# Kernel tuning notes

Hardware: AMD Instinct MI355X
Metric: run time of the kernel (lower is better)

Reference implementation:

```python
import jax, jax.numpy as jnp
import numpy as np

B, T, N, D = 8, 64, 128, 128  # batch, timesteps, num_nodes, hidden_dim
LN_EPS = 1e-5
L2_EPS = 1e-12


def setup_inputs() -> dict:
    key = jax.random.key(0)
    ks = jax.random.split(key, 8)
    feat = jax.random.normal(ks[0], (B, T, N, D), dtype=jnp.float32)
    w = jax.random.uniform(ks[1], (D,), dtype=jnp.float32)  # learned adj gate (torch.rand init)
    s = 1.0 / np.sqrt(D)
    W1 = jax.random.uniform(ks[2], (D, D), dtype=jnp.float32, minval=-s, maxval=s)
    b1 = jax.random.uniform(ks[3], (D,), dtype=jnp.float32, minval=-s, maxval=s)
    W2 = jax.random.uniform(ks[4], (D, D), dtype=jnp.float32, minval=-s, maxval=s)
    b2 = jax.random.uniform(ks[5], (D,), dtype=jnp.float32, minval=-s, maxval=s)
    gamma = jnp.ones((D,), dtype=jnp.float32)
    beta = jnp.zeros((D,), dtype=jnp.float32)
    return {"feat": feat, "w": w, "W1": W1, "b1": b1, "W2": W2, "b2": b2,
            "gamma": gamma, "beta": beta}


def _windows(x):
    # x: (B, T, N, D) -> (B, T-2, 3*N, D): 3 consecutive timesteps flattened over nodes
    b, t, n, d = x.shape
    return jnp.stack([x[:, i:i + t - 2] for i in range(3)], axis=2).reshape(b, t - 2, 3 * n, d)


def reference(feat, w, W1, b1, W2, b2, gamma, beta):
    # gated + L2-normalized features for learned adjacency
    wf = feat * jax.nn.sigmoid(w)
    wf = wf / jnp.maximum(jnp.linalg.norm(wf, axis=-1, keepdims=True), L2_EPS)

    win = _windows(feat)   # (B, T-2, 3N, D)
    wwin = _windows(wf)    # (B, T-2, 3N, D)

    # learned adjacency: gram matrix per window, (B, T-2, 3N, 3N)
    adj = jnp.einsum('btmd,btnd->btmn', wwin, wwin)

    # symmetric normalization D^{-1/2} A D^{-1/2}; inf/nan (deg<=0) -> 0 as in torch
    deg = adj.sum(axis=-1, keepdims=True)
    dis = jnp.where(deg > 0, jax.lax.rsqrt(jnp.maximum(deg, 1e-38)), 0.0)
    nadj = dis * adj * jnp.swapaxes(dis, -1, -2)

    # message passing, keep last N rows (current timestep)
    agg = jnp.einsum('btmn,btnd->btmd', nadj, win)[:, :, -N:, :]

    # FFN (dropout is identity in eval): Linear -> ReLU -> Linear
    h = jax.nn.relu(agg @ W1 + b1) @ W2 + b2

    # residual with current-timestep features + LayerNorm
    s = feat[:, 2:] + h
    mu = s.mean(axis=-1, keepdims=True)
    var = ((s - mu) ** 2).mean(axis=-1, keepdims=True)
    return (s - mu) * jax.lax.rsqrt(var + LN_EPS) * gamma + beta
```

## Files before the change

### kernel.cpp

```cpp
#include <hip/hip_runtime.h>
#include <math.h>

#define BB    8
#define TDIM  64
#define NN    128
#define DD    128
#define TTOUT 62
#define W3    384
#define LG    136
#define LP    40
#define LW    72

typedef __attribute__((ext_vector_type(8))) short bf16x8;
typedef __attribute__((ext_vector_type(4))) float f32x4;

__device__ __forceinline__ float sigf(float x){ return 1.0f/(1.0f+__expf(-x)); }
__device__ __forceinline__ unsigned short f2bf(float x){
  union{float f; unsigned u;} v; v.f=x;
  unsigned r = v.u + 0x7FFFu + ((v.u>>16)&1u);
  return (unsigned short)(r>>16);
}

__global__ void k_rscale(const float* __restrict__ feat, const float* __restrict__ w,
                         float* __restrict__ rscale){
  int row  = blockIdx.x*4 + (threadIdx.x>>6);
  int lane = threadIdx.x & 63;
  float2 f  = *(const float2*)(feat + (size_t)row*DD + lane*2);
  float2 wv = *(const float2*)(w + lane*2);
  float v0 = f.x * sigf(wv.x);
  float v1 = f.y * sigf(wv.y);
  float ss = v0*v0 + v1*v1;
  #pragma unroll
  for(int k=32;k>=1;k>>=1) ss += __shfl_xor(ss, k);
  if(lane==0) rscale[row] = 1.0f / fmaxf(sqrtf(ss), 1e-12f);
}

__global__ void k_ssum(const float* __restrict__ feat, const float* __restrict__ w,
                       const float* __restrict__ rscale, float* __restrict__ ssum){
  int bt = blockIdx.x;
  int d  = threadIdx.x;
  const float* fp = feat + (size_t)bt*NN*DD + d;
  const float* rp = rscale + bt*NN;
  float acc = 0.f;
  #pragma unroll 4
  for(int n=0;n<NN;n++) acc += fp[(size_t)n*DD] * rp[n];
  ssum[bt*DD + d] = acc * sigf(w[d]);
}

__global__ void k_dis(const float* __restrict__ feat, const float* __restrict__ w,
                      const float* __restrict__ rscale, const float* __restrict__ ssum,
                      float* __restrict__ dis){
  __shared__ float s3[DD];
  __shared__ float sg[DD];
  int bt2 = blockIdx.x;
  int b = bt2 / TTOUT, tt = bt2 % TTOUT;
  int tid = threadIdx.x;
  if(tid < DD){
    int base = (b*TDIM + tt)*DD;
    s3[tid] = ssum[base+tid] + ssum[base+DD+tid] + ssum[base+2*DD+tid];
    sg[tid] = sigf(w[tid]);
  }
  __syncthreads();
  int gr = (b*TDIM + tt)*NN + tid;
  const float4* fr = (const float4*)(feat + (size_t)gr*DD);
  float deg = 0.f;
  #pragma unroll 8
  for(int q=0;q<DD/4;q++){
    float4 f = fr[q];
    deg += f.x*sg[q*4+0]*s3[q*4+0] + f.y*sg[q*4+1]*s3[q*4+1]
         + f.z*sg[q*4+2]*s3[q*4+2] + f.w*sg[q*4+3]*s3[q*4+3];
  }
  deg *= rscale[gr];
  dis[(size_t)bt2*W3 + tid] = (deg > 0.f) ? rsqrtf(fmaxf(deg, 1e-38f)) : 0.f;
}

__global__ __launch_bounds__(512,4) void k_main(
    const float* __restrict__ feat,
    const float* __restrict__ W1, const float* __restrict__ b1,
    const float* __restrict__ W2, const float* __restrict__ b2,
    const float* __restrict__ gamma, const float* __restrict__ beta,
    const float* __restrict__ w,
    const float* __restrict__ rscale, const float* __restrict__ dis,
    float* __restrict__ out)
{
  __shared__ __align__(16) unsigned short sm[32000];
  __shared__ float sSig[DD];
  unsigned short* sA  = sm;
  unsigned short* sG  = sm + 17408;
  unsigned short* sFt = sm + 21760;
  unsigned short* sP  = sm + 26880;
  unsigned short* sWt = sm + 17408;

  const int bt2 = blockIdx.x;
  const int tid = threadIdx.x;
  const int rowBase = (bt2/TTOUT)*TDIM*NN + (bt2%TTOUT)*NN;
  const float* disP = dis + (size_t)bt2*W3;

  const int lane = tid & 63, wid = tid >> 6;
  const int l15 = lane & 15, l4 = lane >> 4;
  const int m0 = wid * 16;

  if(tid < DD) sSig[tid] = sigf(w[tid]);
  __syncthreads();

  #pragma unroll
  for(int e0=0; e0<8; ++e0){
    int e = e0*512 + tid;
    int d = e & 127, r0 = (e>>7)*4;
    float sg = sSig[d];
    #pragma unroll
    for(int i=0;i<4;i++){
      int j = 256 + r0 + i, gr = rowBase + j;
      float f = feat[(size_t)gr*DD + d];
      float fac = rscale[gr]*disP[j];
      sA[(r0+i)*LG + d] = f2bf(f*sg*fac);
    }
  }

  f32x4 acc2[8];
  #pragma unroll
  for(int i=0;i<8;i++) acc2[i] = (f32x4){0.f,0.f,0.f,0.f};

  for(int c=0; c<12; ++c){
    const int n0 = c*32;
    __syncthreads();
    #pragma unroll
    for(int e0=0; e0<2; ++e0){
      int e = e0*512 + tid;
      int d = e & 127, r0 = (e>>7)*4;
      float sg = sSig[d];
      unsigned short fb[4];
      #pragma unroll
      for(int i=0;i<4;i++){
        int j = n0 + r0 + i, gr = rowBase + j;
        float f = feat[(size_t)gr*DD + d];
        float fac = rscale[gr]*disP[j];
        fb[i] = f2bf(f);
        sG[(r0+i)*LG + d] = f2bf(f*sg*fac);
      }
      unsigned int* fp = (unsigned int*)&sFt[d*LP + r0];
      fp[0] = (unsigned)fb[0] | ((unsigned)fb[1]<<16);
      fp[1] = (unsigned)fb[2] | ((unsigned)fb[3]<<16);
    }
    __syncthreads();

    f32x4 p0 = {0.f,0.f,0.f,0.f}, p1 = {0.f,0.f,0.f,0.f};
    #pragma unroll
    for(int ks=0; ks<4; ++ks){
      bf16x8 aA  = *(const bf16x8*)&sA[(m0+l15)*LG + ks*32 + l4*8];
      bf16x8 bg0 = *(const bf16x8*)&sG[( 0+l15)*LG + ks*32 + l4*8];
      bf16x8 bg1 = *(const bf16x8*)&sG[(16+l15)*LG + ks*32 + l4*8];
      p0 = __builtin_amdgcn_mfma_f32_16x16x32_bf16(aA, bg0, p0, 0,0,0);
      p1 = __builtin_amdgcn_mfma_f32_16x16x32_bf16(aA, bg1, p1, 0,0,0);
    }
    #pragma unroll
    for(int r=0;r<4;r++){
      sP[(m0 + l4*4 + r)*LP +  0 + l15] = f2bf(p0[r]);
      sP[(m0 + l4*4 + r)*LP + 16 + l15] = f2bf(p1[r]);
    }
    __syncthreads();

    bf16x8 aP = *(const bf16x8*)&sP[(m0+l15)*LP + l4*8];
    #pragma unroll
    for(int dt=0; dt<8; ++dt){
      bf16x8 bF = *(const bf16x8*)&sFt[(dt*16+l15)*LP + l4*8];
      acc2[dt] = __builtin_amdgcn_mfma_f32_16x16x32_bf16(aP, bF, acc2[dt], 0,0,0);
    }
  }

  #pragma unroll
  for(int dt=0; dt<8; ++dt)
    #pragma unroll
    for(int r=0;r<4;r++)
      sA[(m0+l4*4+r)*LG + dt*16+l15] = f2bf(acc2[dt][r]);

  f32x4 acch[8];
  #pragma unroll
  for(int dt=0; dt<8; ++dt){
    float bv = b1[dt*16+l15];
    acch[dt] = (f32x4){bv,bv,bv,bv};
  }
  for(int kh=0; kh<2; ++kh){
    __syncthreads();
    #pragma unroll
    for(int e0=0; e0<4; ++e0){
      int e = e0*512+tid;
      int n = e&127, k0 = (e>>7)*4;
      float w0 = W1[(size_t)(kh*64+k0+0)*DD + n];
      float w1v= W1[(size_t)(kh*64+k0+1)*DD + n];
      float w2v= W1[(size_t)(kh*64+k0+2)*DD + n];
      float w3v= W1[(size_t)(kh*64+k0+3)*DD + n];
      unsigned int* wp = (unsigned int*)&sWt[n*LW + k0];
      wp[0] = (unsigned)f2bf(w0) | ((unsigned)f2bf(w1v)<<16);
      wp[1] = (unsigned)f2bf(w2v)| ((unsigned)f2bf(w3v)<<16);
    }
    __syncthreads();
    #pragma unroll
    for(int ks=0; ks<2; ++ks){
      bf16x8 aA = *(const bf16x8*)&sA[(m0+l15)*LG + kh*64 + ks*32 + l4*8];
      #pragma unroll
      for(int dt=0; dt<8; ++dt){
        bf16x8 bW = *(const bf16x8*)&sWt[(dt*16+l15)*LW + ks*32 + l4*8];
        acch[dt] = __builtin_amdgcn_mfma_f32_16x16x32_bf16(aA, bW, acch[dt], 0,0,0);
      }
    }
  }
  __syncthreads();
  #pragma unroll
  for(int dt=0; dt<8; ++dt)
    #pragma unroll
    for(int r=0;r<4;r++)
      sA[(m0+l4*4+r)*LG + dt*16+l15] = f2bf(fmaxf(acch[dt][r], 0.f));

  f32x4 acco[8];
  #pragma unroll
  for(int dt=0; dt<8; ++dt){
    float bv = b2[dt*16+l15];
    acco[dt] = (f32x4){bv,bv,bv,bv};
  }
  for(int kh=0; kh<2; ++kh){
    __syncthreads();
    #pragma unroll
    for(int e0=0; e0<4; ++e0){
      int e = e0*512+tid;
      int n = e&127, k0 = (e>>7)*4;
      float w0 = W2[(size_t)(kh*64+k0+0)*DD + n];
      float w1v= W2[(size_t)(kh*64+k0+1)*DD + n];
      float w2v= W2[(size_t)(kh*64+k0+2)*DD + n];
      float w3v= W2[(size_t)(kh*64+k0+3)*DD + n];
      unsigned int* wp = (unsigned int*)&sWt[n*LW + k0];
      wp[0] = (unsigned)f2bf(w0) | ((unsigned)f2bf(w1v)<<16);
      wp[1] = (unsigned)f2bf(w2v)| ((unsigned)f2bf(w3v)<<16);
    }
    __syncthreads();
    #pragma unroll
    for(int ks=0; ks<2; ++ks){
      bf16x8 aA = *(const bf16x8*)&sA[(m0+l15)*LG + kh*64 + ks*32 + l4*8];
      #pragma unroll
      for(int dt=0; dt<8; ++dt){
        bf16x8 bW = *(const bf16x8*)&sWt[(dt*16+l15)*LW + ks*32 + l4*8];
        acco[dt] = __builtin_amdgcn_mfma_f32_16x16x32_bf16(aA, bW, acco[dt], 0,0,0);
      }
    }
  }

  const float* fres = feat + (size_t)(rowBase + 256)*DD;
  #pragma unroll
  for(int r=0;r<4;r++){
    int m = m0 + l4*4 + r;
    float vals[8]; float s1 = 0.f, s2 = 0.f;
    #pragma unroll
    for(int dt=0; dt<8; ++dt){
      int d = dt*16 + l15;
      float v = acco[dt][r] + fres[(size_t)m*DD + d];
      vals[dt] = v; s1 += v; s2 += v*v;
    }
    #pragma unroll
    for(int k=1;k<16;k<<=1){ s1 += __shfl_xor(s1,k); s2 += __shfl_xor(s2,k); }
    float mu   = s1*(1.0f/DD);
    float rstd = rsqrtf(s2*(1.0f/DD) - mu*mu + 1e-5f);
    #pragma unroll
    for(int dt=0; dt<8; ++dt){
      int d = dt*16 + l15;
      out[((size_t)bt2*NN + m)*DD + d] = (vals[dt]-mu)*rstd*gamma[d] + beta[d];
    }
  }
}

extern "C" void kernel_launch(void* const* d_in, const int* in_sizes, int n_in,
                              void* d_out, int out_size, void* d_ws, size_t ws_size,
                              hipStream_t stream){
  const float* feat  = (const float*)d_in[0];
  const float* w     = (const float*)d_in[1];
  const float* W1    = (const float*)d_in[2];
  const float* b1    = (const float*)d_in[3];
  const float* W2    = (const float*)d_in[4];
  const float* b2    = (const float*)d_in[5];
  const float* gamma = (const float*)d_in[6];
  const float* beta  = (const float*)d_in[7];
  float* out = (float*)d_out;

  float* rscale = (float*)d_ws;
  float* ssum   = rscale + BB*TDIM*NN;
  float* dis    = ssum   + BB*TDIM*DD;

  k_rscale<<<BB*TDIM*NN/4, 256, 0, stream>>>(feat, w, rscale);
  k_ssum  <<<BB*TDIM,      128, 0, stream>>>(feat, w, rscale, ssum);
  k_dis   <<<BB*TTOUT,     W3,  0, stream>>>(feat, w, rscale, ssum, dis);
  k_main  <<<BB*TTOUT,     512, 0, stream>>>(feat, W1, b1, W2, b2, gamma, beta, w,
                                             rscale, dis, out);
}
```

Measured before the change: 90.92 us.

## Precompute bf16 normalized features and transposed weights; defer degree scaling to Gram output

A fused preprocessing kernel computes the L2 scale, per-timestep column sums and bf16 copies of the gated-normalized features and the raw features in one pass. A separate kernel pre-transposes W1/W2 to bf16, and per-row degree partials over five neighbouring timesteps replace the per-window degree kernel. The main kernel now loads the bf16 tiles with vectorized copies instead of recomputing and converting per element, and applies the D^-1/2 scaling to the Gram block output rather than to the inputs. This adds workspace traffic and extra launches but cuts redundant recomputation across the overlapping windows, at the cost of slightly different rounding.

```diff
diff --git a/kernel.cpp b/kernel.cpp
--- a/kernel.cpp
+++ b/kernel.cpp
@@ -8,7 +8,8 @@
 #define TTOUT 62
 #define W3    384
 #define LG    136
-#define LP    40
+#define LPF   44
+#define LPP   44
 #define LW    72
 
 typedef __attribute__((ext_vector_type(8))) short bf16x8;
@@ -21,100 +22,151 @@
   return (unsigned short)(r>>16);
 }
 
-__global__ void k_rscale(const float* __restrict__ feat, const float* __restrict__ w,
-                         float* __restrict__ rscale){
-  int row  = blockIdx.x*4 + (threadIdx.x>>6);
-  int lane = threadIdx.x & 63;
-  float2 f  = *(const float2*)(feat + (size_t)row*DD + lane*2);
-  float2 wv = *(const float2*)(w + lane*2);
-  float v0 = f.x * sigf(wv.x);
-  float v1 = f.y * sigf(wv.y);
-  float ss = v0*v0 + v1*v1;
-  #pragma unroll
-  for(int k=32;k>=1;k>>=1) ss += __shfl_xor(ss, k);
-  if(lane==0) rscale[row] = 1.0f / fmaxf(sqrtf(ss), 1e-12f);
-}
-
-__global__ void k_ssum(const float* __restrict__ feat, const float* __restrict__ w,
-                       const float* __restrict__ rscale, float* __restrict__ ssum){
-  int bt = blockIdx.x;
-  int d  = threadIdx.x;
-  const float* fp = feat + (size_t)bt*NN*DD + d;
-  const float* rp = rscale + bt*NN;
-  float acc = 0.f;
-  #pragma unroll 4
-  for(int n=0;n<NN;n++) acc += fp[(size_t)n*DD] * rp[n];
-  ssum[bt*DD + d] = acc * sigf(w[d]);
-}
-
-__global__ void k_dis(const float* __restrict__ feat, const float* __restrict__ w,
-                      const float* __restrict__ rscale, const float* __restrict__ ssum,
-                      float* __restrict__ dis){
-  __shared__ float s3[DD];
-  __shared__ float sg[DD];
-  int bt2 = blockIdx.x;
-  int b = bt2 / TTOUT, tt = bt2 % TTOUT;
-  int tid = threadIdx.x;
+template<bool FBF>
+__global__ __launch_bounds__(512) void k_pre(const float* __restrict__ feat,
+    const float* __restrict__ w, unsigned short* __restrict__ gbf,
+    unsigned short* __restrict__ fbf, float* __restrict__ rscale,
+    float* __restrict__ ssum){
+  __shared__ float sSig[DD];
+  __shared__ float sPart[8*DD];
+  const int bt = blockIdx.x, tid = threadIdx.x;
+  if(tid < DD) sSig[tid] = sigf(w[tid]);
+  __syncthreads();
+  const int row = tid >> 2, q = tid & 3;
+  const float* fp = feat + ((size_t)bt*NN + row)*DD + q*32;
+  float f[32], g[32];
+  #pragma unroll
+  for(int i=0;i<8;i++){
+    float4 v = *(const float4*)(fp + i*4);
+    f[i*4]=v.x; f[i*4+1]=v.y; f[i*4+2]=v.z; f[i*4+3]=v.w;
+  }
+  float ss = 0.f;
+  #pragma unroll
+  for(int j=0;j<32;j++){ g[j] = f[j]*sSig[q*32+j]; ss += g[j]*g[j]; }
+  ss += __shfl_xor(ss,1); ss += __shfl_xor(ss,2);
+  float rs = 1.0f / fmaxf(sqrtf(ss), 1e-12f);
+  if(q==0) rscale[(size_t)bt*NN + row] = rs;
+  #pragma unroll
+  for(int j=0;j<32;j++) g[j] *= rs;
+  {
+    unsigned u[16];
+    #pragma unroll
+    for(int j=0;j<16;j++) u[j] = (unsigned)f2bf(g[2*j]) | ((unsigned)f2bf(g[2*j+1])<<16);
+    uint4* dst = (uint4*)(gbf + ((size_t)bt*NN+row)*DD + q*32);
+    #pragma unroll
+    for(int i=0;i<4;i++) dst[i] = *(uint4*)&u[i*4];
+  }
+  if(FBF){
+    unsigned u[16];
+    #pragma unroll
+    for(int j=0;j<16;j++) u[j] = (unsigned)f2bf(f[2*j]) | ((unsigned)f2bf(f[2*j+1])<<16);
+    uint4* dst = (uint4*)(fbf + ((size_t)bt*NN+row)*DD + q*32);
+    #pragma unroll
+    for(int i=0;i<4;i++) dst[i] = *(uint4*)&u[i*4];
+  }
+  #pragma unroll
+  for(int k=4;k<64;k<<=1){
+    #pragma unroll
+    for(int j=0;j<32;j++) g[j] += __shfl_xor(g[j], k);
+  }
+  const int lane = tid & 63, wid = tid >> 6;
+  if((lane>>2)==0){
+    #pragma unroll
+    for(int j=0;j<32;j++) sPart[wid*DD + q*32 + j] = g[j];
+  }
+  __syncthreads();
   if(tid < DD){
-    int base = (b*TDIM + tt)*DD;
-    s3[tid] = ssum[base+tid] + ssum[base+DD+tid] + ssum[base+2*DD+tid];
-    sg[tid] = sigf(w[tid]);
+    float s = 0.f;
+    #pragma unroll
+    for(int wv=0; wv<8; wv++) s += sPart[wv*DD + tid];
+    ssum[(size_t)bt*DD + tid] = s;
+  }
+}
+
+__global__ void k_wt(const float* __restrict__ W1, const float* __restrict__ W2,
+                     unsigned short* __restrict__ W1T, unsigned short* __restrict__ W2T){
+  int k = blockIdx.x & 127, m = blockIdx.x >> 7;
+  int n = threadIdx.x;
+  const float* W = m ? W2 : W1;
+  unsigned short* WT = m ? W2T : W1T;
+  WT[n*DD + k] = f2bf(W[(size_t)k*DD + n]);
+}
+
+__global__ __launch_bounds__(256) void k_d5(const float* __restrict__ feat,
+    const float* __restrict__ w, const float* __restrict__ rscale,
+    const float* __restrict__ ssum, float* __restrict__ d5){
+  __shared__ float s5[5*DD];
+  const int tb = blockIdx.x, tid = threadIdx.x;
+  for(int e=tid; e<5*DD; e+=256){
+    int k = e>>7, d = e&127;
+    int t2 = (tb & 63) - 2 + k;
+    float v = 0.f;
+    if(t2 >= 0 && t2 < TDIM) v = sigf(w[d]) * ssum[(size_t)(tb + k - 2)*DD + d];
+    s5[k*DD + d] = v;
   }
   __syncthreads();
-  int gr = (b*TDIM + tt)*NN + tid;
-  const float4* fr = (const float4*)(feat + (size_t)gr*DD);
-  float deg = 0.f;
-  #pragma unroll 8
-  for(int q=0;q<DD/4;q++){
-    float4 f = fr[q];
-    deg += f.x*sg[q*4+0]*s3[q*4+0] + f.y*sg[q*4+1]*s3[q*4+1]
-         + f.z*sg[q*4+2]*s3[q*4+2] + f.w*sg[q*4+3]*s3[q*4+3];
-  }
-  deg *= rscale[gr];
-  dis[(size_t)bt2*W3 + tid] = (deg > 0.f) ? rsqrtf(fmaxf(deg, 1e-38f)) : 0.f;
-}
-
+  const int row = tid>>1, h = tid&1;
+  const float* fp = feat + ((size_t)tb*NN + row)*DD + h*64;
+  float a0=0,a1=0,a2=0,a3=0,a4=0;
+  #pragma unroll
+  for(int i=0;i<16;i++){
+    float4 v = *(const float4*)(fp + i*4);
+    const float* s0 = s5 + h*64 + i*4;
+    a0 += v.x*s0[0*DD+0] + v.y*s0[0*DD+1] + v.z*s0[0*DD+2] + v.w*s0[0*DD+3];
+    a1 += v.x*s0[1*DD+0] + v.y*s0[1*DD+1] + v.z*s0[1*DD+2] + v.w*s0[1*DD+3];
+    a2 += v.x*s0[2*DD+0] + v.y*s0[2*DD+1] + v.z*s0[2*DD+2] + v.w*s0[2*DD+3];
+    a3 += v.x*s0[3*DD+0] + v.y*s0[3*DD+1] + v.z*s0[3*DD+2] + v.w*s0[3*DD+3];
+    a4 += v.x*s0[4*DD+0] + v.y*s0[4*DD+1] + v.z*s0[4*DD+2] + v.w*s0[4*DD+3];
+  }
+  a0 += __shfl_xor(a0,1); a1 += __shfl_xor(a1,1); a2 += __shfl_xor(a2,1);
+  a3 += __shfl_xor(a3,1); a4 += __shfl_xor(a4,1);
+  if(h==0){
+    float rs = rscale[(size_t)tb*NN + row];
+    float* dp = d5 + ((size_t)tb*NN + row)*5;
+    dp[0]=a0*rs; dp[1]=a1*rs; dp[2]=a2*rs; dp[3]=a3*rs; dp[4]=a4*rs;
+  }
+}
+
+template<bool FBF>
 __global__ __launch_bounds__(512,4) void k_main(
     const float* __restrict__ feat,
-    const float* __restrict__ W1, const float* __restrict__ b1,
-    const float* __restrict__ W2, const float* __restrict__ b2,
+    const unsigned short* __restrict__ gbf,
+    const unsigned short* __restrict__ fbf,
+    const float* __restrict__ d5,
+    const unsigned short* __restrict__ W1T, const float* __restrict__ b1,
+    const unsigned short* __restrict__ W2T, const float* __restrict__ b2,
     const float* __restrict__ gamma, const float* __restrict__ beta,
-    const float* __restrict__ w,
-    const float* __restrict__ rscale, const float* __restrict__ dis,
     float* __restrict__ out)
 {
-  __shared__ __align__(16) unsigned short sm[32000];
-  __shared__ float sSig[DD];
+  __shared__ __align__(16) unsigned short sm[33024];
+  __shared__ float sDis[W3];
   unsigned short* sA  = sm;
   unsigned short* sG  = sm + 17408;
   unsigned short* sFt = sm + 21760;
-  unsigned short* sP  = sm + 26880;
+  unsigned short* sP  = sm + 27392;
   unsigned short* sWt = sm + 17408;
 
   const int bt2 = blockIdx.x;
   const int tid = threadIdx.x;
   const int rowBase = (bt2/TTOUT)*TDIM*NN + (bt2%TTOUT)*NN;
-  const float* disP = dis + (size_t)bt2*W3;
 
   const int lane = tid & 63, wid = tid >> 6;
   const int l15 = lane & 15, l4 = lane >> 4;
   const int m0 = wid * 16;
 
-  if(tid < DD) sSig[tid] = sigf(w[tid]);
-  __syncthreads();
-
-  #pragma unroll
-  for(int e0=0; e0<8; ++e0){
-    int e = e0*512 + tid;
-    int d = e & 127, r0 = (e>>7)*4;
-    float sg = sSig[d];
-    #pragma unroll
-    for(int i=0;i<4;i++){
-      int j = 256 + r0 + i, gr = rowBase + j;
-      float f = feat[(size_t)gr*DD + d];
-      float fac = rscale[gr]*disP[j];
-      sA[(r0+i)*LG + d] = f2bf(f*sg*fac);
-    }
+  if(tid < W3){
+    int jb = tid >> 7;
+    const float* dp = d5 + (size_t)(rowBase + tid)*5 + (2 - jb);
+    float deg = dp[0] + dp[1] + dp[2];
+    sDis[tid] = (deg > 0.f) ? rsqrtf(fmaxf(deg, 1e-38f)) : 0.f;
+  }
+
+  #pragma unroll
+  for(int it=0; it<4; ++it){
+    int e = it*512 + tid;
+    int r = e >> 4, sg = e & 15;
+    uint4 v = *(const uint4*)(gbf + (size_t)(rowBase+256+r)*DD + sg*8);
+    *(uint4*)(sA + r*LG + sg*8) = v;
   }
 
   f32x4 acc2[8];
@@ -124,23 +176,37 @@
   for(int c=0; c<12; ++c){
     const int n0 = c*32;
     __syncthreads();
-    #pragma unroll
-    for(int e0=0; e0<2; ++e0){
-      int e = e0*512 + tid;
-      int d = e & 127, r0 = (e>>7)*4;
-      float sg = sSig[d];
-      unsigned short fb[4];
-      #pragma unroll
-      for(int i=0;i<4;i++){
-        int j = n0 + r0 + i, gr = rowBase + j;
-        float f = feat[(size_t)gr*DD + d];
-        float fac = rscale[gr]*disP[j];
-        fb[i] = f2bf(f);
-        sG[(r0+i)*LG + d] = f2bf(f*sg*fac);
+    {
+      int r = tid >> 4, sg = tid & 15;
+      uint4 v = *(const uint4*)(gbf + (size_t)(rowBase+n0+r)*DD + sg*8);
+      *(uint4*)(sG + r*LG + sg*8) = v;
+    }
+    {
+      int p = tid & 63, rg = tid >> 6;
+      int d0 = p*2, r0 = rg*4;
+      unsigned v0,v1,v2,v3;
+      if(FBF){
+        v0 = *(const unsigned*)(fbf + (size_t)(rowBase+n0+r0+0)*DD + d0);
+        v1 = *(const unsigned*)(fbf + (size_t)(rowBase+n0+r0+1)*DD + d0);
+        v2 = *(const unsigned*)(fbf + (size_t)(rowBase+n0+r0+2)*DD + d0);
+        v3 = *(const unsigned*)(fbf + (size_t)(rowBase+n0+r0+3)*DD + d0);
+      } else {
+        float2 a0 = *(const float2*)(feat + (size_t)(rowBase+n0+r0+0)*DD + d0);
+        float2 a1 = *(const float2*)(feat + (size_t)(rowBase+n0+r0+1)*DD + d0);
+        float2 a2 = *(const float2*)(feat + (size_t)(rowBase+n0+r0+2)*DD + d0);
+        float2 a3 = *(const float2*)(feat + (size_t)(rowBase+n0+r0+3)*DD + d0);
+        v0 = (unsigned)f2bf(a0.x) | ((unsigned)f2bf(a0.y)<<16);
+        v1 = (unsigned)f2bf(a1.x) | ((unsigned)f2bf(a1.y)<<16);
+        v2 = (unsigned)f2bf(a2.x) | ((unsigned)f2bf(a2.y)<<16);
+        v3 = (unsigned)f2bf(a3.x) | ((unsigned)f2bf(a3.y)<<16);
       }
-      unsigned int* fp = (unsigned int*)&sFt[d*LP + r0];
-      fp[0] = (unsigned)fb[0] | ((unsigned)fb[1]<<16);
-      fp[1] = (unsigned)fb[2] | ((unsigned)fb[3]<<16);
+      uint2 lo, hi;
+      lo.x = (v0 & 0xffffu) | (v1 << 16);
+      lo.y = (v2 & 0xffffu) | (v3 << 16);
+      hi.x = (v0 >> 16) | (v1 & 0xffff0000u);
+      hi.y = (v2 >> 16) | (v3 & 0xffff0000u);
+      *(uint2*)(sFt + (size_t)d0*LPF + r0)     = lo;
+      *(uint2*)(sFt + (size_t)(d0+1)*LPF + r0) = hi;
     }
     __syncthreads();
 
@@ -153,17 +219,21 @@
       p0 = __builtin_amdgcn_mfma_f32_16x16x32_bf16(aA, bg0, p0, 0,0,0);
       p1 = __builtin_amdgcn_mfma_f32_16x16x32_bf16(aA, bg1, p1, 0,0,0);
     }
-    #pragma unroll
-    for(int r=0;r<4;r++){
-      sP[(m0 + l4*4 + r)*LP +  0 + l15] = f2bf(p0[r]);
-      sP[(m0 + l4*4 + r)*LP + 16 + l15] = f2bf(p1[r]);
-    }
-    __syncthreads();
-
-    bf16x8 aP = *(const bf16x8*)&sP[(m0+l15)*LP + l4*8];
+    {
+      float dn0 = sDis[n0 + l15], dn1 = sDis[n0 + 16 + l15];
+      #pragma unroll
+      for(int r=0;r<4;r++){
+        float dm = sDis[256 + m0 + l4*4 + r];
+        sP[(m0+l4*4+r)*LPP +  0 + l15] = f2bf(p0[r]*dm*dn0);
+        sP[(m0+l4*4+r)*LPP + 16 + l15] = f2bf(p1[r]*dm*dn1);
+      }
+    }
+    __syncthreads();
+
+    bf16x8 aP = *(const bf16x8*)&sP[(m0+l15)*LPP + l4*8];
     #pragma unroll
     for(int dt=0; dt<8; ++dt){
-      bf16x8 bF = *(const bf16x8*)&sFt[(dt*16+l15)*LP + l4*8];
+      bf16x8 bF = *(const bf16x8*)&sFt[(dt*16+l15)*LPF + l4*8];
       acc2[dt] = __builtin_amdgcn_mfma_f32_16x16x32_bf16(aP, bF, acc2[dt], 0,0,0);
     }
   }
@@ -183,16 +253,11 @@
   for(int kh=0; kh<2; ++kh){
     __syncthreads();
     #pragma unroll
-    for(int e0=0; e0<4; ++e0){
-      int e = e0*512+tid;
-      int n = e&127, k0 = (e>>7)*4;
-      float w0 = W1[(size_t)(kh*64+k0+0)*DD + n];
-      float w1v= W1[(size_t)(kh*64+k0+1)*DD + n];
-      float w2v= W1[(size_t)(kh*64+k0+2)*DD + n];
-      float w3v= W1[(size_t)(kh*64+k0+3)*DD + n];
-      unsigned int* wp = (unsigned int*)&sWt[n*LW + k0];
-      wp[0] = (unsigned)f2bf(w0) | ((unsigned)f2bf(w1v)<<16);
-      wp[1] = (unsigned)f2bf(w2v)| ((unsigned)f2bf(w3v)<<16);
+    for(int it=0; it<2; ++it){
+      int e = it*512 + tid;
+      int n = e>>3, sg = e&7;
+      uint4 v = *(const uint4*)(W1T + (size_t)n*DD + kh*64 + sg*8);
+      *(uint4*)(sWt + n*LW + sg*8) = v;
     }
     __syncthreads();
     #pragma unroll
@@ -221,16 +286,11 @@
   for(int kh=0; kh<2; ++kh){
     __syncthreads();
     #pragma unroll
-    for(int e0=0; e0<4; ++e0){
-      int e = e0*512+tid;
-      int n = e&127, k0 = (e>>7)*4;
-      float w0 = W2[(size_t)(kh*64+k0+0)*DD + n];
-      float w1v= W2[(size_t)(kh*64+k0+1)*DD + n];
-      float w2v= W2[(size_t)(kh*64+k0+2)*DD + n];
-      float w3v= W2[(size_t)(kh*64+k0+3)*DD + n];
-      unsigned int* wp = (unsigned int*)&sWt[n*LW + k0];
-      wp[0] = (unsigned)f2bf(w0) | ((unsigned)f2bf(w1v)<<16);
-      wp[1] = (unsigned)f2bf(w2v)| ((unsigned)f2bf(w3v)<<16);
+    for(int it=0; it<2; ++it){
+      int e = it*512 + tid;
+      int n = e>>3, sg = e&7;
+      uint4 v = *(const uint4*)(W2T + (size_t)n*DD + kh*64 + sg*8);
+      *(uint4*)(sWt + n*LW + sg*8) = v;
     }
     __syncthreads();
     #pragma unroll
@@ -280,13 +340,20 @@
   const float* beta  = (const float*)d_in[7];
   float* out = (float*)d_out;
 
-  float* rscale = (float*)d_ws;
-  float* ssum   = rscale + BB*TDIM*NN;
-  float* dis    = ssum   + BB*TDIM*DD;
-
-  k_rscale<<<BB*TDIM*NN/4, 256, 0, stream>>>(feat, w, rscale);
-  k_ssum  <<<BB*TDIM,      128, 0, stream>>>(feat, w, rscale, ssum);
-  k_dis   <<<BB*TTOUT,     W3,  0, stream>>>(feat, w, rscale, ssum, dis);
-  k_main  <<<BB*TTOUT,     512, 0, stream>>>(feat, W1, b1, W2, b2, gamma, beta, w,
-                                             rscale, dis, out);
-}
+  char* ws = (char*)d_ws;
+  unsigned short* gbf = (unsigned short*)ws;
+  float* rscale = (float*)(ws + 16777216);
+  float* ssum   = (float*)(ws + 17039360);
+  float* d5     = (float*)(ws + 17301504);
+  unsigned short* W1T = (unsigned short*)(ws + 18612224);
+  unsigned short* W2T = (unsigned short*)(ws + 18644992);
+  unsigned short* fbf = (unsigned short*)(ws + 18677760);
+  const bool useF = (ws_size >= (size_t)35454976);
+
+  if(useF) k_pre<true ><<<BB*TDIM, 512, 0, stream>>>(feat, w, gbf, fbf, rscale, ssum);
+  else     k_pre<false><<<BB*TDIM, 512, 0, stream>>>(feat, w, gbf, nullptr, rscale, ssum);
+  k_wt<<<256, 128, 0, stream>>>(W1, W2, W1T, W2T);
+  k_d5<<<BB*TDIM, 256, 0, stream>>>(feat, w, rscale, ssum, d5);
+  if(useF) k_main<true ><<<BB*TTOUT, 512, 0, stream>>>(feat, gbf, fbf, d5, W1T, b1, W2T, b2, gamma, beta, out);
+  else     k_main<false><<<BB*TTOUT, 512, 0, stream>>>(feat, gbf, nullptr, d5, W1T, b1, W2T, b2, gamma, beta, out);
+}
```

New measurement: 116.6 us (median of 4 runs). +28.3%, slower.

## Fuse rscale and ssum passes, pre-transpose weights to bf16, remap block order

Applied to the files above, without the earlier changes.

Merges the row-norm and column-sum prepasses into one kernel that reads each feature tile once, using shuffles and shared memory for the reductions. Two extra blocks transpose W1/W2 into bf16 in the workspace, so the main kernel copies them with 16-byte vector loads instead of converting fp32 elements per block. The main kernel also remaps block index to batch-interleaved order, which may change L2 locality. The cost is a heavier register footprint in the prepass and a dependence on the workspace layout.

```diff
diff --git a/kernel.cpp b/kernel.cpp
--- a/kernel.cpp
+++ b/kernel.cpp
@@ -21,30 +21,58 @@
   return (unsigned short)(r>>16);
 }
 
-__global__ void k_rscale(const float* __restrict__ feat, const float* __restrict__ w,
-                         float* __restrict__ rscale){
-  int row  = blockIdx.x*4 + (threadIdx.x>>6);
-  int lane = threadIdx.x & 63;
-  float2 f  = *(const float2*)(feat + (size_t)row*DD + lane*2);
-  float2 wv = *(const float2*)(w + lane*2);
-  float v0 = f.x * sigf(wv.x);
-  float v1 = f.y * sigf(wv.y);
-  float ss = v0*v0 + v1*v1;
-  #pragma unroll
-  for(int k=32;k>=1;k>>=1) ss += __shfl_xor(ss, k);
-  if(lane==0) rscale[row] = 1.0f / fmaxf(sqrtf(ss), 1e-12f);
-}
-
-__global__ void k_ssum(const float* __restrict__ feat, const float* __restrict__ w,
-                       const float* __restrict__ rscale, float* __restrict__ ssum){
-  int bt = blockIdx.x;
-  int d  = threadIdx.x;
-  const float* fp = feat + (size_t)bt*NN*DD + d;
-  const float* rp = rscale + bt*NN;
-  float acc = 0.f;
-  #pragma unroll 4
-  for(int n=0;n<NN;n++) acc += fp[(size_t)n*DD] * rp[n];
-  ssum[bt*DD + d] = acc * sigf(w[d]);
+__global__ __launch_bounds__(512) void k_pre(const float* __restrict__ feat,
+    const float* __restrict__ w, const float* __restrict__ W1, const float* __restrict__ W2,
+    float* __restrict__ rscale, float* __restrict__ ssum,
+    unsigned short* __restrict__ W1T, unsigned short* __restrict__ W2T){
+  __shared__ float sSig[DD];
+  __shared__ float sPart[8*DD];
+  const int bid = blockIdx.x, tid = threadIdx.x;
+  if(bid >= BB*TDIM){
+    const float* W = (bid == BB*TDIM) ? W1 : W2;
+    unsigned short* WT = (bid == BB*TDIM) ? W1T : W2T;
+    for(int e=tid; e<DD*DD; e+=512){
+      int k = e>>7, n = e&127;
+      WT[n*DD + k] = f2bf(W[(size_t)k*DD + n]);
+    }
+    return;
+  }
+  const int bt = bid;
+  if(tid < DD) sSig[tid] = sigf(w[tid]);
+  __syncthreads();
+  const int row = tid >> 2, q = tid & 3;
+  const float* fp = feat + ((size_t)bt*NN + row)*DD + q*32;
+  float g[32];
+  #pragma unroll
+  for(int i=0;i<8;i++){
+    float4 v = *(const float4*)(fp + i*4);
+    g[i*4]=v.x; g[i*4+1]=v.y; g[i*4+2]=v.z; g[i*4+3]=v.w;
+  }
+  float ss = 0.f;
+  #pragma unroll
+  for(int j=0;j<32;j++){ g[j] *= sSig[q*32+j]; ss += g[j]*g[j]; }
+  ss += __shfl_xor(ss,1); ss += __shfl_xor(ss,2);
+  float rs = 1.0f / fmaxf(sqrtf(ss), 1e-12f);
+  if(q==0) rscale[(size_t)bt*NN + row] = rs;
+  #pragma unroll
+  for(int j=0;j<32;j++) g[j] *= rs;
+  #pragma unroll
+  for(int k=4;k<64;k<<=1){
+    #pragma unroll
+    for(int j=0;j<32;j++) g[j] += __shfl_xor(g[j], k);
+  }
+  const int lane = tid & 63, wid = tid >> 6;
+  if((lane>>2)==0){
+    #pragma unroll
+    for(int j=0;j<32;j++) sPart[wid*DD + q*32 + j] = g[j];
+  }
+  __syncthreads();
+  if(tid < DD){
+    float s = 0.f;
+    #pragma unroll
+    for(int wv=0; wv<8; wv++) s += sPart[wv*DD + tid];
+    ssum[(size_t)bt*DD + tid] = s;
+  }
 }
 
 __global__ void k_dis(const float* __restrict__ feat, const float* __restrict__ w,
@@ -76,11 +104,11 @@
 
 __global__ __launch_bounds__(512,4) void k_main(
     const float* __restrict__ feat,
-    const float* __restrict__ W1, const float* __restrict__ b1,
-    const float* __restrict__ W2, const float* __restrict__ b2,
-    const float* __restrict__ gamma, const float* __restrict__ beta,
     const float* __restrict__ w,
     const float* __restrict__ rscale, const float* __restrict__ dis,
+    const unsigned short* __restrict__ W1T, const float* __restrict__ b1,
+    const unsigned short* __restrict__ W2T, const float* __restrict__ b2,
+    const float* __restrict__ gamma, const float* __restrict__ beta,
     float* __restrict__ out)
 {
   __shared__ __align__(16) unsigned short sm[32000];
@@ -91,8 +119,9 @@
   unsigned short* sP  = sm + 26880;
   unsigned short* sWt = sm + 17408;
 
-  const int bt2 = blockIdx.x;
   const int tid = threadIdx.x;
+  const int bid = blockIdx.x;
+  const int bt2 = (bid & 7)*62 + (bid >> 3);
   const int rowBase = (bt2/TTOUT)*TDIM*NN + (bt2%TTOUT)*NN;
   const float* disP = dis + (size_t)bt2*W3;
 
@@ -183,16 +212,10 @@
   for(int kh=0; kh<2; ++kh){
     __syncthreads();
     #pragma unroll
-    for(int e0=0; e0<4; ++e0){
-      int e = e0*512+tid;
-      int n = e&127, k0 = (e>>7)*4;
-      float w0 = W1[(size_t)(kh*64+k0+0)*DD + n];
-      float w1v= W1[(size_t)(kh*64+k0+1)*DD + n];
-      float w2v= W1[(size_t)(kh*64+k0+2)*DD + n];
-      float w3v= W1[(size_t)(kh*64+k0+3)*DD + n];
-      unsigned int* wp = (unsigned int*)&sWt[n*LW + k0];
-      wp[0] = (unsigned)f2bf(w0) | ((unsigned)f2bf(w1v)<<16);
-      wp[1] = (unsigned)f2bf(w2v)| ((unsigned)f2bf(w3v)<<16);
+    for(int it=0; it<2; ++it){
+      int e = it*512 + tid, n = e>>3, sg2 = e&7;
+      uint4 v = *(const uint4*)(W1T + (size_t)n*DD + kh*64 + sg2*8);
+      *(uint4*)(sWt + n*LW + sg2*8) = v;
     }
     __syncthreads();
     #pragma unroll
@@ -221,16 +244,10 @@
   for(int kh=0; kh<2; ++kh){
     __syncthreads();
     #pragma unroll
-    for(int e0=0; e0<4; ++e0){
-      int e = e0*512+tid;
-      int n = e&127, k0 = (e>>7)*4;
-      float w0 = W2[(size_t)(kh*64+k0+0)*DD + n];
-      float w1v= W2[(size_t)(kh*64+k0+1)*DD + n];
-      float w2v= W2[(size_t)(kh*64+k0+2)*DD + n];
-      float w3v= W2[(size_t)(kh*64+k0+3)*DD + n];
-      unsigned int* wp = (unsigned int*)&sWt[n*LW + k0];
-      wp[0] = (unsigned)f2bf(w0) | ((unsigned)f2bf(w1v)<<16);
-      wp[1] = (unsigned)f2bf(w2v)| ((unsigned)f2bf(w3v)<<16);
+    for(int it=0; it<2; ++it){
+      int e = it*512 + tid, n = e>>3, sg2 = e&7;
+      uint4 v = *(const uint4*)(W2T + (size_t)n*DD + kh*64 + sg2*8);
+      *(uint4*)(sWt + n*LW + sg2*8) = v;
     }
     __syncthreads();
     #pragma unroll
@@ -280,13 +297,15 @@
   const float* beta  = (const float*)d_in[7];
   float* out = (float*)d_out;
 
-  float* rscale = (float*)d_ws;
-  float* ssum   = rscale + BB*TDIM*NN;
-  float* dis    = ssum   + BB*TDIM*DD;
-
-  k_rscale<<<BB*TDIM*NN/4, 256, 0, stream>>>(feat, w, rscale);
-  k_ssum  <<<BB*TDIM,      128, 0, stream>>>(feat, w, rscale, ssum);
-  k_dis   <<<BB*TTOUT,     W3,  0, stream>>>(feat, w, rscale, ssum, dis);
-  k_main  <<<BB*TTOUT,     512, 0, stream>>>(feat, W1, b1, W2, b2, gamma, beta, w,
-                                             rscale, dis, out);
-}
+  char* ws = (char*)d_ws;
+  float* rscale = (float*)(ws + 0);
+  float* ssum   = (float*)(ws + 262144);
+  float* dis    = (float*)(ws + 524288);
+  unsigned short* W1T = (unsigned short*)(ws + 1286144);
+  unsigned short* W2T = (unsigned short*)(ws + 1318912);
+
+  k_pre<<<BB*TDIM + 2, 512, 0, stream>>>(feat, w, W1, W2, rscale, ssum, W1T, W2T);
+  k_dis<<<BB*TTOUT, W3, 0, stream>>>(feat, w, rscale, ssum, dis);
+  k_main<<<BB*TTOUT, 512, 0, stream>>>(feat, w, rscale, dis, W1T, b1, W2T, b2,
+                                       gamma, beta, out);
+}
```

Measured after the change: 89.82 us. No clear change (-1.2%).
